# Kernel tuning notes

Measured on AMD Instinct MI355X. Metric: run time of the kernel, lower is better.

Reference implementation:

```python
import jax, jax.numpy as jnp
import numpy as np

FP4_VALUES = jnp.array([0.0, 0.5, 1.0, 1.5, 2.0, 3.0, 4.0, 6.0,
                        -0.0, -0.5, -1.0, -1.5, -2.0, -3.0, -4.0, -6.0], dtype=jnp.float32)
ALPHA = 1.702
LIMIT = 7.0


def convert_moe_packed_tensors(blocks, scales):
    """Dequantize MXFP4: blocks [E, R, G, 16] packed nibbles, scales [E, R, G] biased exponents.
    Returns [E, G*32, R] fp32 (transposed like the torch reference)."""
    lo = FP4_VALUES[blocks & 0x0F]          # even output positions
    hi = FP4_VALUES[(blocks >> 4) & 0x0F]   # odd output positions
    vals = jnp.stack([lo, hi], axis=-1).reshape(*blocks.shape[:-1], 32)  # [E,R,G,32] interleaved
    scale = jnp.exp2((scales - 127).astype(jnp.float32))                 # 2**(s-127)
    w = vals * scale[..., None]
    E, R = blocks.shape[0], blocks.shape[1]
    return w.reshape(E, R, -1).transpose(0, 2, 1)  # [E, G*32, R]


def setup_inputs() -> dict:
    key = jax.random.key(0)
    ks = jax.random.split(key, 8)
    E, H, I = 8, 2880, 2880
    B, S = 1, 1024
    hidden_states = jax.random.normal(ks[0], (B, S, H), dtype=jnp.float32)
    routing_weights = jax.random.uniform(ks[1], (B * S, E), dtype=jnp.float32)
    gate_up_proj_blocks = jax.random.randint(ks[2], (E, 2 * I, H // 32, 16), 0, 256, dtype=jnp.int32)
    gate_up_proj_scales = jax.random.randint(ks[3], (E, 2 * I, H // 32), 118, 130, dtype=jnp.int32)
    gate_up_proj_bias = jax.random.normal(ks[4], (E, 2 * I), dtype=jnp.float32)
    down_proj_blocks = jax.random.randint(ks[5], (E, H, I // 32, 16), 0, 256, dtype=jnp.int32)
    down_proj_scales = jax.random.randint(ks[6], (E, H, I // 32), 118, 130, dtype=jnp.int32)
    down_proj_bias = jax.random.normal(ks[7], (E, H), dtype=jnp.float32)
    return {
        "hidden_states": hidden_states,
        "routing_weights": routing_weights,
        "gate_up_proj_blocks": gate_up_proj_blocks,
        "gate_up_proj_scales": gate_up_proj_scales,
        "gate_up_proj_bias": gate_up_proj_bias,
        "down_proj_blocks": down_proj_blocks,
        "down_proj_scales": down_proj_scales,
        "down_proj_bias": down_proj_bias,
    }


def reference(hidden_states, routing_weights, gate_up_proj_blocks, gate_up_proj_scales,
              gate_up_proj_bias, down_proj_blocks, down_proj_scales, down_proj_bias):
    B, S, H = hidden_states.shape
    gate_up_proj = convert_moe_packed_tensors(gate_up_proj_blocks, gate_up_proj_scales)  # [E, H, 2I]
    down_proj = convert_moe_packed_tensors(down_proj_blocks, down_proj_scales)           # [E, I, H]
    x = hidden_states.reshape(-1, H)                                                     # [T, H]
    # dense all-expert GLU MLP
    gate_up = jnp.einsum('th,ehf->etf', x, gate_up_proj) + gate_up_proj_bias[:, None, :]  # [E, T, 2I]
    gate = jnp.minimum(gate_up[..., ::2], LIMIT)
    up = jnp.clip(gate_up[..., 1::2], -LIMIT, LIMIT)
    glu = gate * jax.nn.sigmoid(gate * ALPHA)
    nxt = jnp.einsum('eti,eih->eth', (up + 1.0) * glu, down_proj) + down_proj_bias[:, None, :]  # [E, T, H]
    nxt = nxt * routing_weights.T[:, :, None]   # weight each expert's output per token
    out = nxt.sum(axis=0).reshape(B, S, H)
    return out
```

## Files before the change

kernel.cpp:

```cpp
#include <hip/hip_runtime.h>
#include <cstdint>


typedef float  floatx4 __attribute__((ext_vector_type(4)));
typedef __bf16 bf16x8  __attribute__((ext_vector_type(8)));

#define E8   8
#define Hdim 2880
#define Idim 2880
#define Ttok 1024
#define R1   5760
#define Gg   90
#define K2   (E8 * Idim)

__device__ __forceinline__ void load_lds16(const void* gptr, void* lptr) {
  __builtin_amdgcn_global_load_lds(
      (const __attribute__((address_space(1))) uint32_t*)gptr,
      (__attribute__((address_space(3))) uint32_t*)lptr, 16, 0, 0);
}

__device__ __forceinline__ uint32_t f2bf(float f) {
  uint32_t u = __float_as_uint(f);
  return (u + 0x7FFFu + ((u >> 16) & 1u)) >> 16;
}

__device__ __forceinline__ uint32_t perm(uint32_t hi, uint32_t lo, uint32_t sel) {
  return __builtin_amdgcn_perm(hi, lo, sel);
}

struct DqLut { uint32_t Ll, Lh, Hl, Hh; };

__device__ __forceinline__ DqLut make_lut(int s) {
  uint32_t A  = ((uint32_t)(s - 127) << 7) & 0xFFFFu;
  uint32_t e1 = (0x3F00u + A) & 0xFFFFu, e2 = (0x3F80u + A) & 0xFFFFu;
  uint32_t e3 = (0x3FC0u + A) & 0xFFFFu, e4 = (0x4000u + A) & 0xFFFFu;
  uint32_t e5 = (0x4040u + A) & 0xFFFFu, e6 = (0x4080u + A) & 0xFFFFu;
  uint32_t e7 = (0x40C0u + A) & 0xFFFFu;
  uint32_t B01 = e1 << 16, B23 = e2 | (e3 << 16);
  uint32_t B45 = e4 | (e5 << 16), B67 = e6 | (e7 << 16);
  DqLut L;
  L.Ll = perm(B23, B01, 0x06040200u);
  L.Hl = perm(B23, B01, 0x07050301u);
  L.Lh = perm(B67, B45, 0x06040200u);
  L.Hh = perm(B67, B45, 0x07050301u);
  return L;
}

__device__ __forceinline__ uint4 dq8(const DqLut& L, int4 wr) {
  uint32_t p = perm((uint32_t)wr.y, (uint32_t)wr.x, 0x04000400u);
  uint32_t q = perm((uint32_t)wr.w, (uint32_t)wr.z, 0x04000400u);
  uint32_t w = perm(q, p, 0x05040100u);
  uint32_t ilo = w & 0x07070707u;
  uint32_t ihi = (w >> 4) & 0x07070707u;
  uint32_t Llo = perm(L.Lh, L.Ll, ilo);
  uint32_t Hlo = perm(L.Hh, L.Hl, ilo) | ((w << 4) & 0x80808080u);
  uint32_t Lhi = perm(L.Lh, L.Ll, ihi);
  uint32_t Hhi = perm(L.Hh, L.Hl, ihi) | (w & 0x80808080u);
  uint32_t t0 = perm(Hlo, Llo, 0x05010400u);
  uint32_t t1 = perm(Hlo, Llo, 0x07030602u);
  uint32_t t2 = perm(Hhi, Lhi, 0x05010400u);
  uint32_t t3 = perm(Hhi, Lhi, 0x07030602u);
  uint4 o;
  o.x = perm(t2, t0, 0x05040100u);
  o.y = perm(t2, t0, 0x07060302u);
  o.z = perm(t3, t1, 0x05040100u);
  o.w = perm(t3, t1, 0x07060302u);
  return o;
}

__global__ void cvt_x_kernel(const float* __restrict__ x, uint16_t* __restrict__ xb, int n) {
  int i = (blockIdx.x * 256 + threadIdx.x) * 4;
  if (i >= n) return;
  float4 v = *(const float4*)(x + i);
  ushort4 o = make_ushort4((uint16_t)f2bf(v.x), (uint16_t)f2bf(v.y),
                           (uint16_t)f2bf(v.z), (uint16_t)f2bf(v.w));
  *(ushort4*)(xb + i) = o;
}

__global__ void dq_w_kernel(const int* __restrict__ blocks, const int* __restrict__ scales,
                            uint16_t* __restrict__ wd) {
  size_t g = (size_t)blockIdx.x * 256 + threadIdx.x;
  const int4* bp = (const int4*)(blocks + g * 16);
  int4 w0 = bp[0], w1 = bp[1], w2 = bp[2], w3 = bp[3];
  DqLut L = make_lut(scales[g]);
  uint4* op = (uint4*)(wd + g * 32);
  op[0] = dq8(L, w0); op[1] = dq8(L, w1); op[2] = dq8(L, w2); op[3] = dq8(L, w3);
}

__global__ void dq_w2t_kernel(const int* __restrict__ blocks, const int* __restrict__ scales,
                              uint16_t* __restrict__ wt) {
  size_t g = (size_t)blockIdx.x * 256 + threadIdx.x;
  int e  = (int)(g / ((size_t)Hdim * Gg));
  int rm = (int)(g % ((size_t)Hdim * Gg));
  int h  = rm / Gg;
  int ig = rm % Gg;
  const int4* bp = (const int4*)(blocks + g * 16);
  int4 w0 = bp[0], w1 = bp[1], w2 = bp[2], w3 = bp[3];
  DqLut L = make_lut(scales[g]);
  uint4* op = (uint4*)(wt + ((size_t)h * E8 + e) * Idim + (size_t)ig * 32);
  op[0] = dq8(L, w0); op[1] = dq8(L, w1); op[2] = dq8(L, w2); op[3] = dq8(L, w3);
}

__global__ void bias_init_kernel(const float* __restrict__ rw, const float* __restrict__ bias,
                                 float* __restrict__ out) {
  int t  = blockIdx.y;
  int h4 = (blockIdx.x * 256 + threadIdx.x) * 4;
  if (h4 >= Hdim) return;
  float4 s = make_float4(0.f, 0.f, 0.f, 0.f);
  #pragma unroll
  for (int e = 0; e < E8; ++e) {
    float w = rw[t * E8 + e];
    float4 b = *(const float4*)(bias + (size_t)e * Hdim + h4);
    s.x += w * b.x; s.y += w * b.y; s.z += w * b.z; s.w += w * b.w;
  }
  *(float4*)(out + (size_t)t * Hdim + h4) = s;
}

__global__ __launch_bounds__(512) void gemm1_dp_kernel(
    const uint16_t* __restrict__ xb, const uint16_t* __restrict__ w1d,
    const float* __restrict__ bias, const float* __restrict__ rw,
    uint16_t* __restrict__ act) {
  extern __shared__ uint16_t smem[];
  uint16_t* sAr = smem;
  uint16_t* sBr = smem + 3 * 8192;
  const int tid  = threadIdx.x;
  const int lane = tid & 63, wv = tid >> 6;
  const int wm = wv >> 1, wn = wv & 1;
  const int col = lane & 15, quad = lane >> 4;
  const int e  = blockIdx.z;
  const int t0 = blockIdx.x * 256;
  const int i0 = blockIdx.y * 64;

  floatx4 acc[4][4] = {};

  const uint16_t* aSrc0;
  const uint16_t* aSrc1;
  const uint16_t* bSrc;
  {
    int L0 = tid;
    int r0 = L0 >> 2;
    int g0 = (L0 & 3) ^ ((r0 >> 1) & 3);
    aSrc0 = xb + (size_t)(t0 + r0) * Hdim + g0 * 8;
    int L1 = 512 + tid;
    int r1 = L1 >> 2;
    int g1 = (L1 & 3) ^ ((r1 >> 1) & 3);
    aSrc1 = xb + (size_t)(t0 + r1) * Hdim + g1 * 8;
    int rb = tid >> 2;
    int gb = (tid & 3) ^ ((rb >> 1) & 3);
    int orig = 2 * (((rb >> 6) << 5) + (rb & 31)) + ((rb >> 5) & 1);
    bSrc = w1d + ((size_t)e * R1 + 2 * i0 + orig) * Hdim + gb * 8;
  }
  const int aOff0 = (wv * 64) * 8;
  const int aOff1 = (512 + wv * 64) * 8;
  const int bOff  = (wv * 64) * 8;

  auto STAGE = [&](int kt, int slot) {
    const int k0 = kt * 32;
    uint16_t* A = sAr + slot * 8192;
    uint16_t* B = sBr + slot * 4096;
    load_lds16(aSrc0 + k0, A + aOff0);
    load_lds16(aSrc1 + k0, A + aOff1);
    load_lds16(bSrc + k0, B + bOff);
  };

  STAGE(0, 0);
  STAGE(1, 1);

  int sr = 0;
  for (int j = 0; j < 90; ++j) {
    asm volatile("s_waitcnt vmcnt(3)" ::: "memory");
    __builtin_amdgcn_s_barrier();
    asm volatile("" ::: "memory");
    int js = j + 2; if (js > 89) js = 89;
    int sw = sr + 2; if (sw >= 3) sw -= 3;
    STAGE(js, sw);

    const uint16_t* A = sAr + sr * 8192;
    const uint16_t* B = sBr + sr * 4096;
    bf16x8 af[4], bfr[4];
    #pragma unroll
    for (int fm = 0; fm < 4; ++fm) {
      int row = wm * 64 + fm * 16 + col;
      int g = quad ^ ((row >> 1) & 3);
      af[fm] = *(const bf16x8*)&A[row * 32 + g * 8];
    }
    #pragma unroll
    for (int fn = 0; fn < 4; ++fn) {
      int row = wn * 64 + fn * 16 + col;
      int g = quad ^ ((row >> 1) & 3);
      bfr[fn] = *(const bf16x8*)&B[row * 32 + g * 8];
    }
    __builtin_amdgcn_s_setprio(1);
    #pragma unroll
    for (int fm = 0; fm < 4; ++fm)
      #pragma unroll
      for (int fn = 0; fn < 4; ++fn)
        acc[fm][fn] = __builtin_amdgcn_mfma_f32_16x16x32_bf16(
            af[fm], bfr[fn], acc[fm][fn], 0, 0, 0);
    __builtin_amdgcn_s_setprio(0);
    sr = (sr + 1 == 3) ? 0 : sr + 1;
  }

  #pragma unroll
  for (int fm = 0; fm < 4; ++fm) {
    #pragma unroll
    for (int p = 0; p < 2; ++p) {
      floatx4 ga = acc[fm][p], ua = acc[fm][p + 2];
      int ig = i0 + wn * 32 + p * 16 + col;
      float bg = bias[(size_t)e * R1 + 2 * ig];
      float bu = bias[(size_t)e * R1 + 2 * ig + 1];
      #pragma unroll
      for (int r = 0; r < 4; ++r) {
        int t = t0 + wm * 64 + fm * 16 + quad * 4 + r;
        float gate = fminf(ga[r] + bg, 7.0f);
        float up   = fminf(fmaxf(ua[r] + bu, -7.0f), 7.0f);
        float glu  = gate / (1.0f + __expf(-1.702f * gate));
        float a    = rw[t * E8 + e] * (up + 1.0f) * glu;
        act[((size_t)t * E8 + e) * Idim + ig] = (uint16_t)f2bf(a);
      }
    }
  }
}

__global__ __launch_bounds__(256) void gemm2_ks_kernel(
    const uint16_t* __restrict__ actT, const uint16_t* __restrict__ w2t,
    float* __restrict__ out) {
  __shared__ uint16_t sA[128 * 64];
  __shared__ uint16_t sB[96 * 64];
  const int tid  = threadIdx.x;
  const int lane = tid & 63, wv = tid >> 6;
  const int wx = wv & 1, wy = wv >> 1;
  const int col = lane & 15, quad = lane >> 4;
  const int t0 = blockIdx.x * 128;
  const int h0 = blockIdx.y * 96;
  const int kbase = blockIdx.z * (K2 / 4);

  floatx4 acc[4][3] = {};

  const uint16_t* aSrc[4];
  uint16_t* aDst[4];
  #pragma unroll
  for (int q = 0; q < 4; ++q) {
    int L = wv * 256 + q * 64 + lane;
    int row = L >> 3;
    int c = (L & 7) ^ (row & 7);
    aSrc[q] = actT + (size_t)(t0 + row) * K2 + kbase + c * 8;
    aDst[q] = &sA[(size_t)(wv * 256 + q * 64) * 8];
  }
  const uint16_t* bSrc[3];
  uint16_t* bDst[3];
  #pragma unroll
  for (int q = 0; q < 3; ++q) {
    int L = wv * 192 + q * 64 + lane;
    int row = L >> 3;
    int c = (L & 7) ^ (row & 7);
    bSrc[q] = w2t + (size_t)(h0 + row) * K2 + kbase + c * 8;
    bDst[q] = &sB[(size_t)(wv * 192 + q * 64) * 8];
  }

  for (int kt = 0; kt < 90; ++kt) {
    __syncthreads();
    const int k0 = kt * 64;
    #pragma unroll
    for (int q = 0; q < 4; ++q) load_lds16(aSrc[q] + k0, aDst[q]);
    #pragma unroll
    for (int q = 0; q < 3; ++q) load_lds16(bSrc[q] + k0, bDst[q]);
    __syncthreads();
    #pragma unroll
    for (int ks = 0; ks < 2; ++ks) {
      bf16x8 af[4], bfr[3];
      #pragma unroll
      for (int fm = 0; fm < 4; ++fm) {
        int row = wy * 64 + fm * 16 + col;
        int c = ((ks << 2) | quad) ^ (row & 7);
        af[fm] = *(const bf16x8*)&sA[row * 64 + c * 8];
      }
      #pragma unroll
      for (int fn = 0; fn < 3; ++fn) {
        int row = wx * 48 + fn * 16 + col;
        int c = ((ks << 2) | quad) ^ (row & 7);
        bfr[fn] = *(const bf16x8*)&sB[row * 64 + c * 8];
      }
      #pragma unroll
      for (int fm = 0; fm < 4; ++fm)
        #pragma unroll
        for (int fn = 0; fn < 3; ++fn)
          acc[fm][fn] = __builtin_amdgcn_mfma_f32_16x16x32_bf16(
              af[fm], bfr[fn], acc[fm][fn], 0, 0, 0);
    }
  }

  #pragma unroll
  for (int fm = 0; fm < 4; ++fm)
    #pragma unroll
    for (int fn = 0; fn < 3; ++fn) {
      int h = h0 + wx * 48 + fn * 16 + col;
      #pragma unroll
      for (int r = 0; r < 4; ++r) {
        int t = t0 + wy * 64 + fm * 16 + quad * 4 + r;
        atomicAdd(out + (size_t)t * Hdim + h, acc[fm][fn][r]);
      }
    }
}

extern "C" void kernel_launch(void* const* d_in, const int* in_sizes, int n_in,
                              void* d_out, int out_size, void* d_ws, size_t ws_size,
                              hipStream_t stream) {
  (void)in_sizes; (void)n_in; (void)out_size; (void)ws_size;
  const float* x        = (const float*)d_in[0];
  const float* rw       = (const float*)d_in[1];
  const int*   gub_b    = (const int*)d_in[2];
  const int*   gub_s    = (const int*)d_in[3];
  const float* gub_bias = (const float*)d_in[4];
  const int*   dwn_b    = (const int*)d_in[5];
  const int*   dwn_s    = (const int*)d_in[6];
  const float* dwn_bias = (const float*)d_in[7];
  float* out = (float*)d_out;

  const size_t nXb  = (size_t)Ttok * Hdim;
  const size_t nAct = (size_t)Ttok * K2;
  const size_t nW1  = (size_t)E8 * R1 * Hdim;

  uint16_t* xb  = (uint16_t*)d_ws;
  uint16_t* act = xb + nXb;
  uint16_t* w1d = act + nAct;
  uint16_t* w2t = w1d + nW1;

  static int attr_set = 0;
  if (!attr_set) {
    (void)hipFuncSetAttribute((const void*)gemm1_dp_kernel,
                              hipFuncAttributeMaxDynamicSharedMemorySize, 73728);
    attr_set = 1;
  }

  cvt_x_kernel<<<dim3((Ttok * Hdim / 4 + 255) / 256), 256, 0, stream>>>(x, xb, Ttok * Hdim);
  dq_w_kernel<<<dim3((int)((size_t)E8 * R1 * Gg / 256)), 256, 0, stream>>>(gub_b, gub_s, w1d);
  dq_w2t_kernel<<<dim3((int)((size_t)E8 * Hdim * Gg / 256)), 256, 0, stream>>>(dwn_b, dwn_s, w2t);
  bias_init_kernel<<<dim3(3, Ttok), 256, 0, stream>>>(rw, dwn_bias, out);
  gemm1_dp_kernel<<<dim3(4, 45, 8), 512, 73728, stream>>>(xb, w1d, gub_bias, rw, act);
  gemm2_ks_kernel<<<dim3(8, 30, 4), 256, 0, stream>>>(act, w2t, out);
}
```

Before: 1.082 ms.

## Triple-buffer gemm2 LDS loads and enlarge tile to 128x128

Rewrites the second GEMM so global-to-LDS loads run through a three-slot ring with K-step 32. Each step issues loads two steps ahead, waits with a partial vmcnt and uses a single barrier, so memory traffic overlaps MFMA work. The output tile grows from 128x96 to 128x128, which raises reuse per loaded byte. Because 2880 is not a multiple of 128, the last tile has clamped row loads and guarded atomics. The change also adds s_setprio around the MFMA block and a new XOR swizzle, at the cost of more LDS and more accumulator registers.

```diff
diff --git a/kernel.cpp b/kernel.cpp
--- a/kernel.cpp
+++ b/kernel.cpp
@@ -222,83 +222,97 @@
   }
 }
 
-__global__ __launch_bounds__(256) void gemm2_ks_kernel(
+__global__ __launch_bounds__(256) void gemm2_dp_kernel(
     const uint16_t* __restrict__ actT, const uint16_t* __restrict__ w2t,
     float* __restrict__ out) {
-  __shared__ uint16_t sA[128 * 64];
-  __shared__ uint16_t sB[96 * 64];
+  __shared__ uint16_t sAr[3][4096];
+  __shared__ uint16_t sBr[3][4096];
   const int tid  = threadIdx.x;
   const int lane = tid & 63, wv = tid >> 6;
-  const int wx = wv & 1, wy = wv >> 1;
+  const int wy = wv >> 1, wx = wv & 1;
   const int col = lane & 15, quad = lane >> 4;
   const int t0 = blockIdx.x * 128;
-  const int h0 = blockIdx.y * 96;
+  const int h0 = blockIdx.y * 128;
   const int kbase = blockIdx.z * (K2 / 4);
 
-  floatx4 acc[4][3] = {};
-
-  const uint16_t* aSrc[4];
-  uint16_t* aDst[4];
-  #pragma unroll
-  for (int q = 0; q < 4; ++q) {
-    int L = wv * 256 + q * 64 + lane;
-    int row = L >> 3;
-    int c = (L & 7) ^ (row & 7);
-    aSrc[q] = actT + (size_t)(t0 + row) * K2 + kbase + c * 8;
-    aDst[q] = &sA[(size_t)(wv * 256 + q * 64) * 8];
-  }
-  const uint16_t* bSrc[3];
-  uint16_t* bDst[3];
-  #pragma unroll
-  for (int q = 0; q < 3; ++q) {
-    int L = wv * 192 + q * 64 + lane;
-    int row = L >> 3;
-    int c = (L & 7) ^ (row & 7);
-    bSrc[q] = w2t + (size_t)(h0 + row) * K2 + kbase + c * 8;
-    bDst[q] = &sB[(size_t)(wv * 192 + q * 64) * 8];
-  }
-
-  for (int kt = 0; kt < 90; ++kt) {
-    __syncthreads();
-    const int k0 = kt * 64;
-    #pragma unroll
-    for (int q = 0; q < 4; ++q) load_lds16(aSrc[q] + k0, aDst[q]);
-    #pragma unroll
-    for (int q = 0; q < 3; ++q) load_lds16(bSrc[q] + k0, bDst[q]);
-    __syncthreads();
-    #pragma unroll
-    for (int ks = 0; ks < 2; ++ks) {
-      bf16x8 af[4], bfr[3];
+  floatx4 acc[4][4] = {};
+
+  const uint16_t* aSrc0; const uint16_t* aSrc1;
+  const uint16_t* bSrc0; const uint16_t* bSrc1;
+  {
+    int L0 = tid;        int r0 = L0 >> 2; int g0 = (L0 & 3) ^ ((r0 >> 1) & 3);
+    aSrc0 = actT + (size_t)(t0 + r0) * K2 + kbase + g0 * 8;
+    int L1 = 256 + tid;  int r1 = L1 >> 2; int g1 = (L1 & 3) ^ ((r1 >> 1) & 3);
+    aSrc1 = actT + (size_t)(t0 + r1) * K2 + kbase + g1 * 8;
+    int M0 = tid;        int s0 = M0 >> 2; int j0 = (M0 & 3) ^ ((s0 >> 1) & 3);
+    int hb0 = h0 + s0; if (hb0 > Hdim - 1) hb0 = Hdim - 1;
+    bSrc0 = w2t + (size_t)hb0 * K2 + kbase + j0 * 8;
+    int M1 = 256 + tid;  int s1 = M1 >> 2; int j1 = (M1 & 3) ^ ((s1 >> 1) & 3);
+    int hb1 = h0 + s1; if (hb1 > Hdim - 1) hb1 = Hdim - 1;
+    bSrc1 = w2t + (size_t)hb1 * K2 + kbase + j1 * 8;
+  }
+  const int off0 = (wv * 64) * 8;
+  const int off1 = 2048 + (wv * 64) * 8;
+
+  auto STAGE = [&](int kt, int slot) {
+    const int k0 = kt * 32;
+    uint16_t* A = &sAr[slot][0];
+    uint16_t* B = &sBr[slot][0];
+    load_lds16(aSrc0 + k0, A + off0);
+    load_lds16(aSrc1 + k0, A + off1);
+    load_lds16(bSrc0 + k0, B + off0);
+    load_lds16(bSrc1 + k0, B + off1);
+  };
+
+  STAGE(0, 0);
+  STAGE(1, 1);
+
+  int sr = 0;
+  for (int j = 0; j < 180; ++j) {
+    asm volatile("s_waitcnt vmcnt(4)" ::: "memory");
+    __builtin_amdgcn_s_barrier();
+    asm volatile("" ::: "memory");
+    int js = j + 2; if (js > 179) js = 179;
+    int sw = sr + 2; if (sw >= 3) sw -= 3;
+    STAGE(js, sw);
+
+    const uint16_t* A = &sAr[sr][0];
+    const uint16_t* B = &sBr[sr][0];
+    bf16x8 af[4], bfr[4];
+    #pragma unroll
+    for (int fm = 0; fm < 4; ++fm) {
+      int row = wy * 64 + fm * 16 + col;
+      int g = quad ^ ((row >> 1) & 3);
+      af[fm] = *(const bf16x8*)&A[row * 32 + g * 8];
+    }
+    #pragma unroll
+    for (int fn = 0; fn < 4; ++fn) {
+      int row = wx * 64 + fn * 16 + col;
+      int g = quad ^ ((row >> 1) & 3);
+      bfr[fn] = *(const bf16x8*)&B[row * 32 + g * 8];
+    }
+    __builtin_amdgcn_s_setprio(1);
+    #pragma unroll
+    for (int fm = 0; fm < 4; ++fm)
       #pragma unroll
-      for (int fm = 0; fm < 4; ++fm) {
-        int row = wy * 64 + fm * 16 + col;
-        int c = ((ks << 2) | quad) ^ (row & 7);
-        af[fm] = *(const bf16x8*)&sA[row * 64 + c * 8];
-      }
-      #pragma unroll
-      for (int fn = 0; fn < 3; ++fn) {
-        int row = wx * 48 + fn * 16 + col;
-        int c = ((ks << 2) | quad) ^ (row & 7);
-        bfr[fn] = *(const bf16x8*)&sB[row * 64 + c * 8];
-      }
-      #pragma unroll
-      for (int fm = 0; fm < 4; ++fm)
-        #pragma unroll
-        for (int fn = 0; fn < 3; ++fn)
-          acc[fm][fn] = __builtin_amdgcn_mfma_f32_16x16x32_bf16(
-              af[fm], bfr[fn], acc[fm][fn], 0, 0, 0);
-    }
+      for (int fn = 0; fn < 4; ++fn)
+        acc[fm][fn] = __builtin_amdgcn_mfma_f32_16x16x32_bf16(
+            af[fm], bfr[fn], acc[fm][fn], 0, 0, 0);
+    __builtin_amdgcn_s_setprio(0);
+    sr = (sr + 1 == 3) ? 0 : sr + 1;
   }
 
   #pragma unroll
   for (int fm = 0; fm < 4; ++fm)
     #pragma unroll
-    for (int fn = 0; fn < 3; ++fn) {
-      int h = h0 + wx * 48 + fn * 16 + col;
-      #pragma unroll
-      for (int r = 0; r < 4; ++r) {
-        int t = t0 + wy * 64 + fm * 16 + quad * 4 + r;
-        atomicAdd(out + (size_t)t * Hdim + h, acc[fm][fn][r]);
+    for (int fn = 0; fn < 4; ++fn) {
+      int h = h0 + wx * 64 + fn * 16 + col;
+      if (h < Hdim) {
+        #pragma unroll
+        for (int r = 0; r < 4; ++r) {
+          int t = t0 + wy * 64 + fm * 16 + quad * 4 + r;
+          atomicAdd(out + (size_t)t * Hdim + h, acc[fm][fn][r]);
+        }
       }
     }
 }
@@ -338,5 +352,5 @@
   dq_w2t_kernel<<<dim3((int)((size_t)E8 * Hdim * Gg / 256)), 256, 0, stream>>>(dwn_b, dwn_s, w2t);
   bias_init_kernel<<<dim3(3, Ttok), 256, 0, stream>>>(rw, dwn_bias, out);
   gemm1_dp_kernel<<<dim3(4, 45, 8), 512, 73728, stream>>>(xb, w1d, gub_bias, rw, act);
-  gemm2_ks_kernel<<<dim3(8, 30, 4), 256, 0, stream>>>(act, w2t, out);
-}
+  gemm2_dp_kernel<<<dim3(8, 23, 4), 256, 0, stream>>>(act, w2t, out);
+}
```

Result: slower. 1.156 ms (+6.9%).
